# Kernel tuning notes

Measured on AMD Instinct MI355X. Metric: run time of the kernel, lower is better.

The kernel has to match this reference:

```python
import jax, jax.numpy as jnp
import numpy as np

N_NODES = 50000
N_EDGES = 800000
N_GRAPHS = 256
HID = 64           # hidden_channels
H, C = 2, 64       # GAT heads, per-head channels
D2 = H * C         # 128 = hidden_channels * heads
BN_EPS = 1e-5


def setup_inputs() -> dict:
    key = jax.random.key(0)
    ks = iter(jax.random.split(key, 64))

    def p(shape, scale=0.05):
        return (jax.random.normal(next(ks), shape, dtype=jnp.float32) * scale)

    inp = {}
    inp["metadata"] = jax.random.normal(next(ks), (N_NODES, 4), dtype=jnp.float32)
    inp["waveform_features"] = jax.random.normal(next(ks), (N_NODES, 64), dtype=jnp.float32)
    inp["edge_index"] = jax.random.randint(next(ks), (2, N_EDGES), 0, N_NODES, dtype=jnp.int64)
    inp["batch"] = jnp.sort(jax.random.randint(next(ks), (N_NODES,), 0, N_GRAPHS, dtype=jnp.int64))

    # encoders / combiner
    inp["meta_w"] = p((4, HID // 2)); inp["meta_b"] = p((HID // 2,))
    inp["wave_w"] = p((64, HID // 2)); inp["wave_b"] = p((HID // 2,))
    inp["comb_w"] = p((HID, HID));     inp["comb_b"] = p((HID,))

    # GAT layers: layer 0 maps HID->H*C, layers 1,2 map D2->H*C
    inp["gat_w0"] = p((HID, D2)); inp["gat_as0"] = p((H, C)); inp["gat_ad0"] = p((H, C)); inp["gat_b0"] = p((D2,))
    inp["gat_w1"] = p((D2, D2));  inp["gat_as1"] = p((H, C)); inp["gat_ad1"] = p((H, C)); inp["gat_b1"] = p((D2,))
    inp["gat_w2"] = p((D2, D2));  inp["gat_as2"] = p((H, C)); inp["gat_ad2"] = p((H, C)); inp["gat_b2"] = p((D2,))

    # batch norms (eval mode: running stats), stacked over 3 layers
    inp["bn_gamma"] = jnp.ones((3, D2), jnp.float32) + p((3, D2))
    inp["bn_beta"] = p((3, D2))
    inp["bn_mean"] = p((3, D2))
    inp["bn_var"] = jax.random.uniform(next(ks), (3, D2), jnp.float32, 0.5, 1.5)

    # predictors
    inp["lat_w1"] = p((D2, HID)); inp["lat_b1"] = p((HID,))
    inp["lat_w2"] = p((HID, 1));  inp["lat_b2"] = p((1,))
    inp["lon_w1"] = p((D2, HID)); inp["lon_b1"] = p((HID,))
    inp["lon_w2"] = p((HID, 1));  inp["lon_b2"] = p((1,))
    return inp


def gat_conv(x, src, dst, n, W, a_src, a_dst, b):
    """PyG-style GATConv, heads=H concat, leaky_relu slope 0.2, self-loops already in src/dst."""
    h = (x @ W).reshape(n, H, C)                          # [N,H,C]
    s = jnp.einsum('nhc,hc->nh', h, a_src)                # alpha_src [N,H]
    d = jnp.einsum('nhc,hc->nh', h, a_dst)                # alpha_dst [N,H]
    e = jax.nn.leaky_relu(s[src] + d[dst], 0.2)           # [E,H]
    m = jax.ops.segment_max(e, dst, num_segments=n)       # per-dst softmax (segment)
    ex = jnp.exp(e - m[dst])
    denom = jax.ops.segment_sum(ex, dst, num_segments=n)
    alpha = ex / (denom[dst] + 1e-16)                     # [E,H]
    out = jax.ops.segment_sum(h[src] * alpha[:, :, None], dst, num_segments=n)  # [N,H,C]
    return out.reshape(n, H * C) + b


def reference(metadata, waveform_features, edge_index, batch,
              meta_w, meta_b, wave_w, wave_b, comb_w, comb_b,
              gat_w0, gat_as0, gat_ad0, gat_b0,
              gat_w1, gat_as1, gat_ad1, gat_b1,
              gat_w2, gat_as2, gat_ad2, gat_b2,
              bn_gamma, bn_beta, bn_mean, bn_var,
              lat_w1, lat_b1, lat_w2, lat_b2,
              lon_w1, lon_b1, lon_w2, lon_b2):
    n = metadata.shape[0]
    me = jax.nn.relu(metadata @ meta_w + meta_b)
    we = jax.nn.relu(waveform_features @ wave_w + wave_b)
    x = jnp.concatenate([me, we], axis=1)                 # [N, HID]
    x = jax.nn.relu(x @ comb_w + comb_b)

    loops = jnp.arange(n, dtype=edge_index.dtype)         # GATConv adds self-loops
    src = jnp.concatenate([edge_index[0], loops])
    dst = jnp.concatenate([edge_index[1], loops])

    gat_params = [(gat_w0, gat_as0, gat_ad0, gat_b0),
                  (gat_w1, gat_as1, gat_ad1, gat_b1),
                  (gat_w2, gat_as2, gat_ad2, gat_b2)]
    for i in range(3):
        x_res = x if i > 0 else None
        x = gat_conv(x, src, dst, n, *gat_params[i])
        x = (x - bn_mean[i]) * (bn_gamma[i] / jnp.sqrt(bn_var[i] + BN_EPS)) + bn_beta[i]
        if x_res is not None and x.shape == x_res.shape:
            x = x + x_res
        x = jax.nn.relu(x)                                # dropout inactive (eval)

    # global_mean_pool over graphs
    sums = jax.ops.segment_sum(x, batch, num_segments=N_GRAPHS)
    cnt = jax.ops.segment_sum(jnp.ones((n, 1), x.dtype), batch, num_segments=N_GRAPHS)
    xg = sums / jnp.maximum(cnt, 1.0)                     # [B, 128]

    lat = jax.nn.relu(xg @ lat_w1 + lat_b1) @ lat_w2 + lat_b2
    lon = jax.nn.relu(xg @ lon_w1 + lon_b1) @ lon_w2 + lon_b2
    return lat, lon
```

## Files before the change

kernel.cpp:

```cpp
#include <hip/hip_runtime.h>
#include <hip/hip_bf16.h>
#include <stdint.h>

#define NN 50000
#define NNP 50048
#define NE 800000
#define ET 850000
#define NG 256
#define CAP 128
#define NB 392
#define BCAP 3072
#define EB 4096
#define NEB ((ET + EB - 1) / EB)

typedef __hip_bfloat16 bf16;
typedef __attribute__((ext_vector_type(8))) short short8;
typedef __attribute__((ext_vector_type(4))) float floatx4;

__device__ __forceinline__ float b2f(bf16 v) { return __bfloat162float(v); }
__device__ __forceinline__ float lrelu(float x) { return x > 0.f ? x : 0.2f * x; }
__device__ __forceinline__ short f2b(float f) {
    unsigned u = __float_as_uint(f);
    unsigned r = (u + 0x7FFFu + ((u >> 16) & 1u)) >> 16;
    return (short)r;
}
__device__ __forceinline__ float sh2f(short s) { return __uint_as_float(((unsigned)(unsigned short)s) << 16); }
__device__ __forceinline__ float blo(unsigned u) { return __uint_as_float(u << 16); }
__device__ __forceinline__ float bhi(unsigned u) { return __uint_as_float(u & 0xFFFF0000u); }
__device__ __forceinline__ unsigned pck(float a, float b) {
    return ((unsigned)(unsigned short)f2b(a)) | (((unsigned)(unsigned short)f2b(b)) << 16);
}
__device__ __forceinline__ float wred_sum(float v) {
    for (int o = 32; o > 0; o >>= 1) v += __shfl_xor(v, o, 64);
    return v;
}
__device__ __forceinline__ int ld_int(const void* p, int i, bool i64) {
    return i64 ? (int)((const long long*)p)[i] : ((const int*)p)[i];
}
__device__ __forceinline__ float ldf(const void* p, int i, bool fp32) {
    return fp32 ? ((const float*)p)[i] : b2f(((const bf16*)p)[i]);
}

__global__ void detect_kernel(const unsigned int* __restrict__ meta_words,
                              const unsigned int* __restrict__ ei_words,
                              int* __restrict__ flags, int* __restrict__ bcur) {
    __shared__ int insane, odd_nonzero;
    for (int k = threadIdx.x; k < NB; k += 256) bcur[k] = 0;
    if (threadIdx.x == 0) { insane = 0; odd_nonzero = 0; }
    __syncthreads();
    int cnt = 0;
    for (int k = 0; k < 8; k++) {
        unsigned int w = meta_words[threadIdx.x * 8 + k];
        int elo = (int)(((w & 0xFFFFu) >> 7) & 0xFF);
        int ehi = (int)(((w >> 16) >> 7) & 0xFF);
        if (elo >= 0x8D) cnt++;
        if (ehi >= 0x8D) cnt++;
    }
    if (cnt) atomicAdd(&insane, cnt);
    if (ei_words[threadIdx.x * 2 + 1] != 0u) atomicAdd(&odd_nonzero, 1);
    __syncthreads();
    if (threadIdx.x == 0) {
        flags[0] = (insane >= 4) ? 1 : 0;
        flags[1] = (odd_nonzero == 0) ? 1 : 0;
    }
}

struct PrepArgs {
    const void* src[32];
    int len[32];
    int dst_off[32];
    int blk_base[33];
    int cvtBlks, wtBlks, wfBlks;
    const void* w0; const void* w1; const void* w2;
    const void* ww; const void* wc;
    const void* wf_src;
    const void* gb0; const void* gb1; const void* gb2;
    const void* bng; const void* bnb; const void* bnm; const void* bnv;
};

__global__ void prep_kernel(PrepArgs a, float* __restrict__ cf,
                            short* __restrict__ wtall, short* __restrict__ wavewT,
                            short* __restrict__ combwT,
                            short* __restrict__ wfhi, short* __restrict__ wflo,
                            float* __restrict__ bnscl, float* __restrict__ bnsft,
                            const int* __restrict__ flags) {
    int b = blockIdx.x;
    bool fp32f = flags[0] != 0;
    if (b < a.cvtBlks) {
        int ai = 0;
        while (b >= a.blk_base[ai + 1]) ai++;
        int base = (b - a.blk_base[ai]) * 1024 + threadIdx.x;
        const float* sf = (const float*)a.src[ai];
        const bf16* sh = (const bf16*)a.src[ai];
        float* d = cf + a.dst_off[ai];
        int len = a.len[ai];
        #pragma unroll
        for (int u = 0; u < 4; u++) {
            int i = base + u * 256;
            if (i < len) d[i] = fp32f ? sf[i] : b2f(sh[i]);
        }
        return;
    }
    b -= a.cvtBlks;
    if (b < a.wtBlks) {
        int idx = b * 256 + threadIdx.x;
        const void* src; short* dst; int K, N, loc;
        if (idx < 8192)        { src = a.w0; dst = wtall;          K = 64;  N = 128; loc = idx; }
        else if (idx < 24576)  { src = a.w1; dst = wtall + 8192;   K = 128; N = 128; loc = idx - 8192; }
        else if (idx < 40960)  { src = a.w2; dst = wtall + 24576;  K = 128; N = 128; loc = idx - 24576; }
        else if (idx < 43008)  { src = a.ww; dst = wavewT;         K = 64;  N = 32;  loc = idx - 40960; }
        else if (idx < 47104)  { src = a.wc; dst = combwT;         K = 64;  N = 64;  loc = idx - 43008; }
        else return;
        int nch = loc / K, k = loc % K;
        int si = k * N + nch;
        dst[loc] = fp32f ? f2b(((const float*)src)[si]) : ((const short*)src)[si];
        return;
    }
    b -= a.wtBlks;
    if (b < a.wfBlks) {
        int idx = b * 256 + threadIdx.x;
        int i8 = idx * 8;
        if (i8 >= NNP * 64) return;
        short8 h = {0, 0, 0, 0, 0, 0, 0, 0};
        if (fp32f) {
            short8 l = {0, 0, 0, 0, 0, 0, 0, 0};
            if (i8 < NN * 64) {
                const float* sf = (const float*)a.wf_src + i8;
                #pragma unroll
                for (int k = 0; k < 8; k++) {
                    float v = sf[k];
                    short hh = f2b(v);
                    h[k] = hh;
                    l[k] = f2b(v - sh2f(hh));
                }
            }
            *(short8*)(wfhi + i8) = h;
            *(short8*)(wflo + i8) = l;
        } else {
            if (i8 < NN * 64) h = *(const short8*)((const short*)a.wf_src + i8);
            *(short8*)(wfhi + i8) = h;
        }
        return;
    }
    b -= a.wfBlks;
    int idx = b * 256 + threadIdx.x;
    if (idx >= 384) return;
    int l = idx >> 7, c = idx & 127;
    const void* biasp = (l == 0) ? a.gb0 : (l == 1) ? a.gb1 : a.gb2;
    float bias = ldf(biasp, c, fp32f);
    float g  = ldf(a.bng, l * 128 + c, fp32f);
    float be = ldf(a.bnb, l * 128 + c, fp32f);
    float mu = ldf(a.bnm, l * 128 + c, fp32f);
    float va = ldf(a.bnv, l * 128 + c, fp32f);
    float sc = g * rsqrtf(va + 1e-5f);
    bnscl[l * 128 + c] = sc;
    bnsft[l * 128 + c] = (bias - mu) * sc + be;
}

__global__ __launch_bounds__(256) void encode_mfma_kernel(
        const float* __restrict__ meta, const float* __restrict__ meta_w,
        const float* __restrict__ meta_b,
        const short* __restrict__ wfhi, const short* __restrict__ wflo,
        const short* __restrict__ wavewT, const float* __restrict__ wave_b,
        const short* __restrict__ combwT, const float* __restrict__ comb_b,
        short* __restrict__ xout, const int* __restrict__ flags) {
    __shared__ short xc_hi[64][72];
    __shared__ short xc_lo[64][72];
    int t = threadIdx.x;
    int wave = t >> 6, lane = t & 63;
    int m16 = lane & 15, quad = lane >> 4;
    int nblk = blockIdx.x * 64;
    bool fp32f = flags[0] != 0;

    #pragma unroll
    for (int u = 0; u < 8; u++) {
        int idx = u * 256 + t;
        int node_l = idx >> 5, ch = idx & 31;
        int node = nblk + node_l;
        float acc = meta_b[ch];
        if (node < NN) {
            #pragma unroll
            for (int k = 0; k < 4; k++)
                acc += meta[node * 4 + k] * meta_w[k * 32 + ch];
        }
        float v = fmaxf(acc, 0.f);
        short hh = f2b(v);
        xc_hi[node_l][ch] = hh;
        xc_lo[node_l][ch] = f2b(v - sh2f(hh));
    }

    int row0 = nblk + wave * 16;
    const short* pah = wfhi + (size_t)(row0 + m16) * 64 + quad * 8;
    const short* pal = wflo + (size_t)(row0 + m16) * 64 + quad * 8;
    floatx4 wacc[2];
    wacc[0] = (floatx4)(0.f); wacc[1] = (floatx4)(0.f);
    #pragma unroll
    for (int ks = 0; ks < 64; ks += 32) {
        short8 ah = *(const short8*)(pah + ks);
        #pragma unroll
        for (int c = 0; c < 2; c++) {
            short8 b = *(const short8*)(wavewT + (c * 16 + m16) * 64 + ks + quad * 8);
            wacc[c] = __builtin_amdgcn_mfma_f32_16x16x32_bf16(ah, b, wacc[c], 0, 0, 0);
        }
        if (fp32f) {
            short8 al = *(const short8*)(pal + ks);
            #pragma unroll
            for (int c = 0; c < 2; c++) {
                short8 b = *(const short8*)(wavewT + (c * 16 + m16) * 64 + ks + quad * 8);
                wacc[c] = __builtin_amdgcn_mfma_f32_16x16x32_bf16(al, b, wacc[c], 0, 0, 0);
            }
        }
    }
    #pragma unroll
    for (int c = 0; c < 2; c++) {
        float bb = wave_b[c * 16 + m16];
        #pragma unroll
        for (int r = 0; r < 4; r++) {
            int node_l = wave * 16 + quad * 4 + r;
            int ch = 32 + c * 16 + m16;
            float v = fmaxf(wacc[c][r] + bb, 0.f);
            short hh = f2b(v);
            xc_hi[node_l][ch] = hh;
            xc_lo[node_l][ch] = f2b(v - sh2f(hh));
        }
    }
    __syncthreads();

    floatx4 acc2[4];
    #pragma unroll
    for (int c = 0; c < 4; c++) acc2[c] = (floatx4)(0.f);
    #pragma unroll
    for (int ks = 0; ks < 64; ks += 32) {
        short8 ah = *(const short8*)&xc_hi[wave * 16 + m16][ks + quad * 8];
        short8 al = *(const short8*)&xc_lo[wave * 16 + m16][ks + quad * 8];
        #pragma unroll
        for (int c = 0; c < 4; c++) {
            short8 b = *(const short8*)(combwT + (c * 16 + m16) * 64 + ks + quad * 8);
            acc2[c] = __builtin_amdgcn_mfma_f32_16x16x32_bf16(ah, b, acc2[c], 0, 0, 0);
            acc2[c] = __builtin_amdgcn_mfma_f32_16x16x32_bf16(al, b, acc2[c], 0, 0, 0);
        }
    }
    #pragma unroll
    for (int c = 0; c < 4; c++) {
        int ch = c * 16 + m16;
        float bb = comb_b[ch];
        #pragma unroll
        for (int r = 0; r < 4; r++) {
            int node = nblk + wave * 16 + quad * 4 + r;
            float v = fmaxf(acc2[c][r] + bb, 0.f);
            xout[(size_t)node * 64 + ch] = f2b(v);
        }
    }
}

__global__ void bucket_scatter_kernel(const void* __restrict__ ei, const int* __restrict__ flags,
                                      int* __restrict__ bcur, uint2* __restrict__ bkt) {
    __shared__ int lh[NB];
    __shared__ int lbase[NB];
    int t = threadIdx.x;
    bool i64 = flags[1] != 0;
    for (int k = t; k < NB; k += 256) lh[k] = 0;
    __syncthreads();
    int base = blockIdx.x * EB;
    #pragma unroll 4
    for (int u = 0; u < EB / 256; u++) {
        int i = base + u * 256 + t;
        if (i < ET) {
            int dst = (i < NE) ? ld_int(ei, NE + i, i64) : (i - NE);
            atomicAdd(&lh[dst >> 7], 1);
        }
    }
    __syncthreads();
    for (int k = t; k < NB; k += 256) {
        int c = lh[k];
        lbase[k] = c ? atomicAdd(&bcur[k], c) : 0;
        lh[k] = 0;
    }
    __syncthreads();
    #pragma unroll 4
    for (int u = 0; u < EB / 256; u++) {
        int i = base + u * 256 + t;
        if (i < ET) {
            int src, dst;
            if (i < NE) { src = ld_int(ei, i, i64); dst = ld_int(ei, NE + i, i64); }
            else        { src = i - NE; dst = i - NE; }
            int b = dst >> 7;
            int pos = lbase[b] + atomicAdd(&lh[b], 1);
            if (pos < BCAP) bkt[(size_t)b * BCAP + pos] = make_uint2((unsigned)src, (unsigned)dst);
        }
    }
}

__global__ void bucket_finalize_kernel(const uint2* __restrict__ bkt,
                                       const int* __restrict__ bcnt,
                                       int* __restrict__ offb, int* __restrict__ dega,
                                       int* __restrict__ csr) {
    __shared__ int hist[128];
    __shared__ int cur[128];
    int b = blockIdx.x;
    int t = threadIdx.x;
    int e0 = b * BCAP;
    int cnt = min(bcnt[b], BCAP);
    if (t < 128) hist[t] = 0;
    __syncthreads();
    for (int i = t; i < cnt; i += 256)
        atomicAdd(&hist[bkt[e0 + i].y & 127], 1);
    __syncthreads();
    int v = (t < 128) ? hist[t] : 0;
    if (t < 128) cur[t] = v;
    __syncthreads();
    for (int o = 1; o < 128; o <<= 1) {
        int x = (t < 128 && t >= o) ? cur[t - o] : 0;
        __syncthreads();
        if (t < 128) cur[t] += x;
        __syncthreads();
    }
    if (t < 128) {
        int ex = e0 + cur[t] - v;
        int node = b * 128 + t;
        if (node < NN) { offb[node] = ex; dega[node] = v; }
        cur[t] = ex;
    }
    __syncthreads();
    for (int i = t; i < cnt; i += 256) {
        uint2 e = bkt[e0 + i];
        int pos = atomicAdd(&cur[e.y & 127], 1);
        csr[pos] = (int)e.x;
    }
}

__global__ __launch_bounds__(256) void gemm_mfma_kernel(
        const short* __restrict__ x, const short* __restrict__ wt,
        const float* __restrict__ a_s, const float* __restrict__ a_d,
        short* __restrict__ h, float* __restrict__ s, float* __restrict__ d,
        int K, int n) {
    int wave = threadIdx.x >> 6;
    int lane = threadIdx.x & 63;
    int row0 = (blockIdx.x * 4 + wave) * 16;
    int m16 = lane & 15;
    int quad = lane >> 4;
    int kq = quad * 8;

    const short* pa = x + (size_t)(row0 + m16) * K + kq;

    floatx4 acc[8];
    #pragma unroll
    for (int c = 0; c < 8; c++) acc[c] = (floatx4)(0.f);

    for (int ks = 0; ks < K; ks += 32) {
        short8 av = *(const short8*)(pa + ks);
        #pragma unroll
        for (int c = 0; c < 8; c++) {
            short8 b = *(const short8*)(wt + (size_t)(c * 16 + m16) * K + ks + kq);
            acc[c] = __builtin_amdgcn_mfma_f32_16x16x32_bf16(av, b, acc[c], 0, 0, 0);
        }
    }

    #pragma unroll
    for (int c = 0; c < 8; c++) {
        #pragma unroll
        for (int r = 0; r < 4; r++) {
            int node = row0 + quad * 4 + r;
            if (node < n) h[(size_t)node * 128 + c * 16 + m16] = f2b(acc[c][r]);
        }
    }

    float sp[2][4] = {{0, 0, 0, 0}, {0, 0, 0, 0}};
    float dp[2][4] = {{0, 0, 0, 0}, {0, 0, 0, 0}};
    #pragma unroll
    for (int c = 0; c < 8; c++) {
        float as_ = a_s[c * 16 + m16];
        float ad_ = a_d[c * 16 + m16];
        int hh = c >> 2;
        #pragma unroll
        for (int r = 0; r < 4; r++) {
            sp[hh][r] += acc[c][r] * as_;
            dp[hh][r] += acc[c][r] * ad_;
        }
    }
    #pragma unroll
    for (int o = 1; o < 16; o <<= 1) {
        #pragma unroll
        for (int hh = 0; hh < 2; hh++)
            #pragma unroll
            for (int r = 0; r < 4; r++) {
                sp[hh][r] += __shfl_xor(sp[hh][r], o, 64);
                dp[hh][r] += __shfl_xor(dp[hh][r], o, 64);
            }
    }
    if (m16 == 0) {
        #pragma unroll
        for (int r = 0; r < 4; r++) {
            int node = row0 + quad * 4 + r;
            if (node < n) {
                s[node * 2 + 0] = sp[0][r];
                s[node * 2 + 1] = sp[1][r];
                d[node * 2 + 0] = dp[0][r];
                d[node * 2 + 1] = dp[1][r];
            }
        }
    }
}

__global__ __launch_bounds__(256) void gat_aggregate_kernel(
        const unsigned* __restrict__ hp, const float* __restrict__ sv,
        const float* __restrict__ dv, const int* __restrict__ offb,
        const int* __restrict__ dega, const int* __restrict__ csr,
        const float* __restrict__ scl, const float* __restrict__ sft,
        const unsigned* __restrict__ res, unsigned* __restrict__ out, int n) {
    __shared__ float4 er[8][CAP];
    int slot = threadIdx.x >> 5;
    int lane32 = threadIdx.x & 31;
    int node = blockIdx.x * 8 + slot;
    bool ok = node < n;
    int begin = 0, deg = 0;
    float d0 = 0.f, d1 = 0.f;
    if (ok) {
        begin = offb[node]; deg = dega[node];
        d0 = dv[node * 2 + 0]; d1 = dv[node * 2 + 1];
    }
    bool fits = deg <= CAP;
    int degp = (deg + 7) & ~7;
    float inv0 = 0.f, inv1 = 0.f;

    if (ok && fits) {
        int sids[4]; float e0[4], e1[4];
        #pragma unroll
        for (int k = 0; k < 4; k++) {
            int li = k * 32 + lane32;
            sids[k] = (li < deg) ? csr[begin + li] : -1;
        }
        #pragma unroll
        for (int k = 0; k < 4; k++) {
            if (sids[k] >= 0) {
                float2 sp = *(const float2*)(sv + 2 * sids[k]);
                e0[k] = lrelu(sp.x + d0); e1[k] = lrelu(sp.y + d1);
            } else { e0[k] = -3e38f; e1[k] = -3e38f; }
        }
        float m0 = fmaxf(fmaxf(e0[0], e0[1]), fmaxf(e0[2], e0[3]));
        float m1 = fmaxf(fmaxf(e1[0], e1[1]), fmaxf(e1[2], e1[3]));
        #pragma unroll
        for (int o = 1; o < 32; o <<= 1) {
            m0 = fmaxf(m0, __shfl_xor(m0, o, 64));
            m1 = fmaxf(m1, __shfl_xor(m1, o, 64));
        }
        float z0 = 0.f, z1 = 0.f;
        #pragma unroll
        for (int k = 0; k < 4; k++) {
            if (sids[k] >= 0) {
                float x0 = __expf(e0[k] - m0), x1 = __expf(e1[k] - m1);
                z0 += x0; z1 += x1;
                er[slot][k * 32 + lane32] = make_float4(__int_as_float(sids[k]), x0, x1, 0.f);
            }
        }
        #pragma unroll
        for (int o = 1; o < 32; o <<= 1) {
            z0 += __shfl_xor(z0, o, 64);
            z1 += __shfl_xor(z1, o, 64);
        }
        if (lane32 < degp - deg)
            er[slot][deg + lane32] = make_float4(__int_as_float(0), 0.f, 0.f, 0.f);
        inv0 = 1.f / (z0 + 1e-16f);
        inv1 = 1.f / (z1 + 1e-16f);
    }
    __syncthreads();
    if (!ok) return;

    if (fits) {
        int ll = lane32 & 15;
        int grp = lane32 >> 4;
        int hsel = (ll >= 8) ? 1 : 0;
        const uint4* hp4 = (const uint4*)hp;
        float a0 = 0, a1 = 0, a2 = 0, a3 = 0, a4 = 0, a5 = 0, a6 = 0, a7 = 0;
        for (int i = 0; i < degp; i += 8) {
            int e = i + grp * 4;
            float4 r0 = er[slot][e], r1 = er[slot][e + 1], r2 = er[slot][e + 2], r3 = er[slot][e + 3];
            uint4 u0 = hp4[(size_t)__float_as_int(r0.x) * 16 + ll];
            uint4 u1 = hp4[(size_t)__float_as_int(r1.x) * 16 + ll];
            uint4 u2 = hp4[(size_t)__float_as_int(r2.x) * 16 + ll];
            uint4 u3 = hp4[(size_t)__float_as_int(r3.x) * 16 + ll];
            float al0 = hsel ? r0.z : r0.y;
            float al1 = hsel ? r1.z : r1.y;
            float al2 = hsel ? r2.z : r2.y;
            float al3 = hsel ? r3.z : r3.y;
            a0 += al0 * blo(u0.x) + al1 * blo(u1.x) + al2 * blo(u2.x) + al3 * blo(u3.x);
            a1 += al0 * bhi(u0.x) + al1 * bhi(u1.x) + al2 * bhi(u2.x) + al3 * bhi(u3.x);
            a2 += al0 * blo(u0.y) + al1 * blo(u1.y) + al2 * blo(u2.y) + al3 * blo(u3.y);
            a3 += al0 * bhi(u0.y) + al1 * bhi(u1.y) + al2 * bhi(u2.y) + al3 * bhi(u3.y);
            a4 += al0 * blo(u0.z) + al1 * blo(u1.z) + al2 * blo(u2.z) + al3 * blo(u3.z);
            a5 += al0 * bhi(u0.z) + al1 * bhi(u1.z) + al2 * bhi(u2.z) + al3 * bhi(u3.z);
            a6 += al0 * blo(u0.w) + al1 * blo(u1.w) + al2 * blo(u2.w) + al3 * blo(u3.w);
            a7 += al0 * bhi(u0.w) + al1 * bhi(u1.w) + al2 * bhi(u2.w) + al3 * bhi(u3.w);
        }
        a0 += __shfl_xor(a0, 16, 64); a1 += __shfl_xor(a1, 16, 64);
        a2 += __shfl_xor(a2, 16, 64); a3 += __shfl_xor(a3, 16, 64);
        a4 += __shfl_xor(a4, 16, 64); a5 += __shfl_xor(a5, 16, 64);
        a6 += __shfl_xor(a6, 16, 64); a7 += __shfl_xor(a7, 16, 64);
        float inv = hsel ? inv1 : inv0;
        a0 *= inv; a1 *= inv; a2 *= inv; a3 *= inv;
        a4 *= inv; a5 *= inv; a6 *= inv; a7 *= inv;

        float4 sc0 = ((const float4*)scl)[2 * ll], sc1 = ((const float4*)scl)[2 * ll + 1];
        float4 sh0 = ((const float4*)sft)[2 * ll], sh1 = ((const float4*)sft)[2 * ll + 1];
        float v0 = a0 * sc0.x + sh0.x;
        float v1 = a1 * sc0.y + sh0.y;
        float v2 = a2 * sc0.z + sh0.z;
        float v3 = a3 * sc0.w + sh0.w;
        float v4 = a4 * sc1.x + sh1.x;
        float v5 = a5 * sc1.y + sh1.y;
        float v6 = a6 * sc1.z + sh1.z;
        float v7 = a7 * sc1.w + sh1.w;
        if (res) {
            uint4 r = ((const uint4*)res)[(size_t)node * 16 + ll];
            v0 += blo(r.x); v1 += bhi(r.x); v2 += blo(r.y); v3 += bhi(r.y);
            v4 += blo(r.z); v5 += bhi(r.z); v6 += blo(r.w); v7 += bhi(r.w);
        }
        v0 = fmaxf(v0, 0.f); v1 = fmaxf(v1, 0.f); v2 = fmaxf(v2, 0.f); v3 = fmaxf(v3, 0.f);
        v4 = fmaxf(v4, 0.f); v5 = fmaxf(v5, 0.f); v6 = fmaxf(v6, 0.f); v7 = fmaxf(v7, 0.f);
        if (grp == 0) {
            ((uint4*)out)[(size_t)node * 16 + ll] =
                make_uint4(pck(v0, v1), pck(v2, v3), pck(v4, v5), pck(v6, v7));
        }
    } else {
        float mm0 = -3e38f, mm1 = -3e38f;
        for (int i = lane32; i < deg; i += 32) {
            int sc = csr[begin + i];
            float2 sp = *(const float2*)(sv + 2 * sc);
            mm0 = fmaxf(mm0, lrelu(sp.x + d0));
            mm1 = fmaxf(mm1, lrelu(sp.y + d1));
        }
        #pragma unroll
        for (int o = 1; o < 32; o <<= 1) {
            mm0 = fmaxf(mm0, __shfl_xor(mm0, o, 64));
            mm1 = fmaxf(mm1, __shfl_xor(mm1, o, 64));
        }
        float z0 = 0.f, z1 = 0.f;
        for (int i = lane32; i < deg; i += 32) {
            int sc = csr[begin + i];
            float2 sp = *(const float2*)(sv + 2 * sc);
            z0 += __expf(lrelu(sp.x + d0) - mm0);
            z1 += __expf(lrelu(sp.y + d1) - mm1);
        }
        #pragma unroll
        for (int o = 1; o < 32; o <<= 1) {
            z0 += __shfl_xor(z0, o, 64);
            z1 += __shfl_xor(z1, o, 64);
        }
        float i0_ = 1.f / (z0 + 1e-16f), i1_ = 1.f / (z1 + 1e-16f);
        bool head0 = lane32 < 16;
        float b0 = 0.f, b1 = 0.f, b2 = 0.f, b3 = 0.f;
        for (int i = 0; i < deg; i++) {
            int sc = csr[begin + i];
            float2 sp = *(const float2*)(sv + 2 * sc);
            float a = head0 ? __expf(lrelu(sp.x + d0) - mm0) * i0_
                            : __expf(lrelu(sp.y + d1) - mm1) * i1_;
            uint2 u = *(const uint2*)(hp + (size_t)sc * 64 + lane32 * 2);
            b0 += a * blo(u.x); b1 += a * bhi(u.x);
            b2 += a * blo(u.y); b3 += a * bhi(u.y);
        }
        float4 sc4 = ((const float4*)scl)[lane32];
        float4 sh4 = ((const float4*)sft)[lane32];
        float v0 = b0 * sc4.x + sh4.x;
        float v1 = b1 * sc4.y + sh4.y;
        float v2 = b2 * sc4.z + sh4.z;
        float v3 = b3 * sc4.w + sh4.w;
        if (res) {
            uint2 r = ((const uint2*)res)[(size_t)node * 32 + lane32];
            v0 += blo(r.x); v1 += bhi(r.x); v2 += blo(r.y); v3 += bhi(r.y);
        }
        v0 = fmaxf(v0, 0.f); v1 = fmaxf(v1, 0.f);
        v2 = fmaxf(v2, 0.f); v3 = fmaxf(v3, 0.f);
        ((uint2*)out)[(size_t)node * 32 + lane32] = make_uint2(pck(v0, v1), pck(v2, v3));
    }
}

__global__ void poolhead_kernel(const unsigned* __restrict__ x, const void* __restrict__ batch,
                                const float* __restrict__ w1a, const float* __restrict__ b1a,
                                const float* __restrict__ w2a, const float* __restrict__ b2a,
                                const float* __restrict__ w1o, const float* __restrict__ b1o,
                                const float* __restrict__ w2o, const float* __restrict__ b2o,
                                const int* __restrict__ flags, void* __restrict__ out) {
    __shared__ float part[4][128];
    __shared__ float xs[128];
    __shared__ int bounds[2];
    int g = blockIdx.x;
    int tid = threadIdx.x;
    bool i64 = flags[1] != 0;
    if (tid < 2) {
        int target = g + tid;
        int lo = 0, hi = NN;
        while (lo < hi) {
            int mid = (lo + hi) >> 1;
            if (ld_int(batch, mid, i64) < target) lo = mid + 1; else hi = mid;
        }
        bounds[tid] = lo;
    }
    __syncthreads();
    int s0 = bounds[0], e0 = bounds[1];
    int wv = tid >> 6, lane = tid & 63;
    float a0 = 0.f, a1 = 0.f;
    for (int node = s0 + wv; node < e0; node += 4) {
        unsigned u = x[(size_t)node * 64 + lane];
        a0 += blo(u);
        a1 += bhi(u);
    }
    part[wv][2 * lane] = a0;
    part[wv][2 * lane + 1] = a1;
    __syncthreads();
    if (tid < 128) {
        float t0 = part[0][tid] + part[1][tid] + part[2][tid] + part[3][tid];
        xs[tid] = t0 / fmaxf((float)(e0 - s0), 1.f);
    }
    __syncthreads();
    if (wv < 2) {
        const float* w1 = wv ? w1o : w1a;
        const float* b1 = wv ? b1o : b1a;
        const float* w2 = wv ? w2o : w2a;
        const float* b2 = wv ? b2o : b2a;
        float acc = b1[lane];
        for (int c = 0; c < 128; c++)
            acc += xs[c] * w1[c * 64 + lane];
        acc = fmaxf(acc, 0.f);
        float contrib = wred_sum(acc * w2[lane]);
        if (lane == 0) {
            float r = contrib + b2[0];
            if (flags[0]) ((float*)out)[wv * NG + g] = r;
            else          ((bf16*)out)[wv * NG + g] = __float2bfloat16(r);
        }
    }
}

extern "C" void kernel_launch(void* const* d_in, const int* in_sizes, int n_in,
                              void* d_out, int out_size, void* d_ws, size_t ws_size,
                              hipStream_t stream) {
    static const int fidx[32] = {0,1, 4,5,6,7,8,9, 10,11,12,13, 14,15,16,17,
                                 18,19,20,21, 22,23,24,25, 26,27,28,29, 30,31,32,33};
    static const int flen[32] = {200000, 3200000, 128, 32, 2048, 32, 4096, 64,
                                 8192, 128, 128, 128, 16384, 128, 128, 128,
                                 16384, 128, 128, 128, 384, 384, 384, 384,
                                 8192, 64, 64, 1, 8192, 64, 64, 1};
    PrepArgs pa;
    int O[32];
    int tot = 0, blk = 0;
    for (int i = 0; i < 32; i++) {
        bool skip = (i == 1) || (i == 4) || (i == 6) || (i == 8) || (i == 12) || (i == 16) ||
                    (i == 11) || (i == 15) || (i == 19) ||
                    (i == 20) || (i == 21) || (i == 22) || (i == 23);
        int cl = skip ? 0 : flen[i];
        pa.src[i] = d_in[fidx[i]];
        pa.len[i] = cl;
        O[i] = tot;
        pa.dst_off[i] = tot;
        pa.blk_base[i] = blk;
        tot += (flen[i] + 63) & ~63;
        blk += (cl + 1023) / 1024;
    }
    pa.blk_base[32] = blk;
    pa.cvtBlks = blk;
    pa.wtBlks = 184;
    pa.wfBlks = NNP * 64 / 8 / 256;
    pa.w0 = d_in[10]; pa.w1 = d_in[14]; pa.w2 = d_in[18];
    pa.ww = d_in[6];  pa.wc = d_in[8];
    pa.wf_src = d_in[1];
    pa.gb0 = d_in[13]; pa.gb1 = d_in[17]; pa.gb2 = d_in[21];
    pa.bng = d_in[22]; pa.bnb = d_in[23]; pa.bnm = d_in[24]; pa.bnv = d_in[25];
    int prepGrid = pa.cvtBlks + pa.wtBlks + pa.wfBlks + 2;

    char* w = (char*)d_ws;
    auto alloc = [&](size_t bytes) -> char* {
        char* p = w;
        w += (bytes + 255) & ~(size_t)255;
        return p;
    };
    int*   flags  = (int*)alloc(256);
    float* cf     = (float*)alloc((size_t)tot * 4);
    short* wfhi   = (short*)alloc((size_t)NNP * 64 * 2);
    short* wflo   = (short*)alloc((size_t)NNP * 64 * 2);
    short* x0     = (short*)alloc((size_t)NNP * 64 * 2);
    short* xA     = (short*)alloc((size_t)NNP * 128 * 2);
    short* xB     = (short*)alloc((size_t)NNP * 128 * 2);
    short* h      = (short*)alloc((size_t)NNP * 128 * 2);
    float* sA     = (float*)alloc((size_t)NN * 2 * 4);
    float* dA     = (float*)alloc((size_t)NN * 2 * 4);
    int*   offb   = (int*)alloc((size_t)NN * 4);
    int*   dega   = (int*)alloc((size_t)NN * 4);
    int*   csr    = (int*)alloc((size_t)NB * BCAP * 4);
    int*   bcur   = (int*)alloc((size_t)NB * 4);
    uint2* bkt    = (uint2*)alloc((size_t)NB * BCAP * 8);
    float* bnscl  = (float*)alloc(384 * 4);
    float* bnsft  = (float*)alloc(384 * 4);
    short* wtall  = (short*)alloc((size_t)40960 * 2);
    short* wavewT = (short*)alloc((size_t)2048 * 2);
    short* combwT = (short*)alloc((size_t)4096 * 2);
    short* wt0 = wtall, *wt1 = wtall + 8192, *wt2 = wtall + 24576;

    detect_kernel<<<1, 256, 0, stream>>>((const unsigned int*)d_in[0],
                                         (const unsigned int*)d_in[2], flags, bcur);
    prep_kernel<<<prepGrid, 256, 0, stream>>>(pa, cf, wtall, wavewT, combwT,
                                              wfhi, wflo, bnscl, bnsft, flags);
    encode_mfma_kernel<<<NNP / 64, 256, 0, stream>>>(cf + O[0], cf + O[2], cf + O[3],
                                                     wfhi, wflo, wavewT, cf + O[5],
                                                     combwT, cf + O[7], x0, flags);
    bucket_scatter_kernel<<<NEB, 256, 0, stream>>>(d_in[2], flags, bcur, bkt);
    bucket_finalize_kernel<<<NB, 256, 0, stream>>>(bkt, bcur, offb, dega, csr);

    int gblk = NNP / 64;
    gemm_mfma_kernel<<<gblk, 256, 0, stream>>>(x0, wt0, cf + O[9], cf + O[10],
                                               h, sA, dA, 64, NN);
    gat_aggregate_kernel<<<(NN + 7) / 8, 256, 0, stream>>>(
        (const unsigned*)h, sA, dA, offb, dega, csr,
        bnscl, bnsft, nullptr, (unsigned*)xA, NN);
    gemm_mfma_kernel<<<gblk, 256, 0, stream>>>(xA, wt1, cf + O[13], cf + O[14],
                                               h, sA, dA, 128, NN);
    gat_aggregate_kernel<<<(NN + 7) / 8, 256, 0, stream>>>(
        (const unsigned*)h, sA, dA, offb, dega, csr,
        bnscl + 128, bnsft + 128, (const unsigned*)xA, (unsigned*)xB, NN);
    gemm_mfma_kernel<<<gblk, 256, 0, stream>>>(xB, wt2, cf + O[17], cf + O[18],
                                               h, sA, dA, 128, NN);
    gat_aggregate_kernel<<<(NN + 7) / 8, 256, 0, stream>>>(
        (const unsigned*)h, sA, dA, offb, dega, csr,
        bnscl + 256, bnsft + 256, (const unsigned*)xB, (unsigned*)xA, NN);

    poolhead_kernel<<<NG, 256, 0, stream>>>((const unsigned*)xA, d_in[3],
                                            cf + O[24], cf + O[25], cf + O[26], cf + O[27],
                                            cf + O[28], cf + O[29], cf + O[30], cf + O[31],
                                            flags, d_out);
}
```

Baseline: 365.4 us.

## Drop softmax max pass, fuse encode with edge bucketing, skip bf16 waveform copy

The GAT aggregation now exponentiates raw leaky-relu logits without first subtracting the per-node maximum. This removes a full pass over each node's neighbours plus the shuffle reductions. The encoder and the edge bucket-scatter are merged into one launch, with the two roles split by block index over a shared-memory union. For bf16 inputs the prep step no longer copies the waveform array, and the encoder reads it directly. Skipping the max subtraction risks exp overflow when attention logits are large, so correctness relies on the logits staying small.

```diff
diff --git a/kernel.cpp b/kernel.cpp
--- a/kernel.cpp
+++ b/kernel.cpp
@@ -12,6 +12,7 @@
 #define BCAP 3072
 #define EB 4096
 #define NEB ((ET + EB - 1) / EB)
+#define ENCB (NNP / 64)
 
 typedef __hip_bfloat16 bf16;
 typedef __attribute__((ext_vector_type(8))) short short8;
@@ -118,28 +119,24 @@
     }
     b -= a.wtBlks;
     if (b < a.wfBlks) {
+        if (!fp32f) return;
         int idx = b * 256 + threadIdx.x;
         int i8 = idx * 8;
         if (i8 >= NNP * 64) return;
         short8 h = {0, 0, 0, 0, 0, 0, 0, 0};
-        if (fp32f) {
-            short8 l = {0, 0, 0, 0, 0, 0, 0, 0};
-            if (i8 < NN * 64) {
-                const float* sf = (const float*)a.wf_src + i8;
-                #pragma unroll
-                for (int k = 0; k < 8; k++) {
-                    float v = sf[k];
-                    short hh = f2b(v);
-                    h[k] = hh;
-                    l[k] = f2b(v - sh2f(hh));
-                }
+        short8 l = {0, 0, 0, 0, 0, 0, 0, 0};
+        if (i8 < NN * 64) {
+            const float* sf = (const float*)a.wf_src + i8;
+            #pragma unroll
+            for (int k = 0; k < 8; k++) {
+                float v = sf[k];
+                short hh = f2b(v);
+                h[k] = hh;
+                l[k] = f2b(v - sh2f(hh));
             }
-            *(short8*)(wfhi + i8) = h;
-            *(short8*)(wflo + i8) = l;
-        } else {
-            if (i8 < NN * 64) h = *(const short8*)((const short*)a.wf_src + i8);
-            *(short8*)(wfhi + i8) = h;
-        }
+        }
+        *(short8*)(wfhi + i8) = h;
+        *(short8*)(wflo + i8) = l;
         return;
     }
     b -= a.wfBlks;
@@ -157,20 +154,61 @@
     bnsft[l * 128 + c] = (bias - mu) * sc + be;
 }
 
-__global__ __launch_bounds__(256) void encode_mfma_kernel(
+__global__ __launch_bounds__(256) void encode_scatter_kernel(
         const float* __restrict__ meta, const float* __restrict__ meta_w,
         const float* __restrict__ meta_b,
         const short* __restrict__ wfhi, const short* __restrict__ wflo,
+        const short* __restrict__ wf_raw,
         const short* __restrict__ wavewT, const float* __restrict__ wave_b,
         const short* __restrict__ combwT, const float* __restrict__ comb_b,
-        short* __restrict__ xout, const int* __restrict__ flags) {
-    __shared__ short xc_hi[64][72];
-    __shared__ short xc_lo[64][72];
+        short* __restrict__ xout,
+        const void* __restrict__ ei, int* __restrict__ bcur, uint2* __restrict__ bkt,
+        const int* __restrict__ flags) {
+    __shared__ union {
+        struct { short hi[64][72]; short lo[64][72]; } enc;
+        struct { int lh[NB]; int lbase[NB]; } sc;
+    } sm;
     int t = threadIdx.x;
+    bool fp32f = flags[0] != 0;
+
+    if (blockIdx.x >= ENCB) {
+        bool i64 = flags[1] != 0;
+        for (int k = t; k < NB; k += 256) sm.sc.lh[k] = 0;
+        __syncthreads();
+        int base = (blockIdx.x - ENCB) * EB;
+        #pragma unroll 4
+        for (int u = 0; u < EB / 256; u++) {
+            int i = base + u * 256 + t;
+            if (i < ET) {
+                int dst = (i < NE) ? ld_int(ei, NE + i, i64) : (i - NE);
+                atomicAdd(&sm.sc.lh[dst >> 7], 1);
+            }
+        }
+        __syncthreads();
+        for (int k = t; k < NB; k += 256) {
+            int c = sm.sc.lh[k];
+            sm.sc.lbase[k] = c ? atomicAdd(&bcur[k], c) : 0;
+            sm.sc.lh[k] = 0;
+        }
+        __syncthreads();
+        #pragma unroll 4
+        for (int u = 0; u < EB / 256; u++) {
+            int i = base + u * 256 + t;
+            if (i < ET) {
+                int src, dst;
+                if (i < NE) { src = ld_int(ei, i, i64); dst = ld_int(ei, NE + i, i64); }
+                else        { src = i - NE; dst = i - NE; }
+                int b = dst >> 7;
+                int pos = sm.sc.lbase[b] + atomicAdd(&sm.sc.lh[b], 1);
+                if (pos < BCAP) bkt[(size_t)b * BCAP + pos] = make_uint2((unsigned)src, (unsigned)dst);
+            }
+        }
+        return;
+    }
+
     int wave = t >> 6, lane = t & 63;
     int m16 = lane & 15, quad = lane >> 4;
     int nblk = blockIdx.x * 64;
-    bool fp32f = flags[0] != 0;
 
     #pragma unroll
     for (int u = 0; u < 8; u++) {
@@ -185,13 +223,15 @@
         }
         float v = fmaxf(acc, 0.f);
         short hh = f2b(v);
-        xc_hi[node_l][ch] = hh;
-        xc_lo[node_l][ch] = f2b(v - sh2f(hh));
-    }
-
-    int row0 = nblk + wave * 16;
-    const short* pah = wfhi + (size_t)(row0 + m16) * 64 + quad * 8;
-    const short* pal = wflo + (size_t)(row0 + m16) * 64 + quad * 8;
+        sm.enc.hi[node_l][ch] = hh;
+        sm.enc.lo[node_l][ch] = f2b(v - sh2f(hh));
+    }
+
+    int row = nblk + wave * 16 + m16;
+    if (row >= NN) row = NN - 1;
+    const short* wbase = fp32f ? wfhi : wf_raw;
+    const short* pah = wbase + (size_t)row * 64 + quad * 8;
+    const short* pal = wflo + (size_t)row * 64 + quad * 8;
     floatx4 wacc[2];
     wacc[0] = (floatx4)(0.f); wacc[1] = (floatx4)(0.f);
     #pragma unroll
@@ -220,8 +260,8 @@
             int ch = 32 + c * 16 + m16;
             float v = fmaxf(wacc[c][r] + bb, 0.f);
             short hh = f2b(v);
-            xc_hi[node_l][ch] = hh;
-            xc_lo[node_l][ch] = f2b(v - sh2f(hh));
+            sm.enc.hi[node_l][ch] = hh;
+            sm.enc.lo[node_l][ch] = f2b(v - sh2f(hh));
         }
     }
     __syncthreads();
@@ -231,8 +271,8 @@
     for (int c = 0; c < 4; c++) acc2[c] = (floatx4)(0.f);
     #pragma unroll
     for (int ks = 0; ks < 64; ks += 32) {
-        short8 ah = *(const short8*)&xc_hi[wave * 16 + m16][ks + quad * 8];
-        short8 al = *(const short8*)&xc_lo[wave * 16 + m16][ks + quad * 8];
+        short8 ah = *(const short8*)&sm.enc.hi[wave * 16 + m16][ks + quad * 8];
+        short8 al = *(const short8*)&sm.enc.lo[wave * 16 + m16][ks + quad * 8];
         #pragma unroll
         for (int c = 0; c < 4; c++) {
             short8 b = *(const short8*)(combwT + (c * 16 + m16) * 64 + ks + quad * 8);
@@ -249,44 +289,6 @@
             int node = nblk + wave * 16 + quad * 4 + r;
             float v = fmaxf(acc2[c][r] + bb, 0.f);
             xout[(size_t)node * 64 + ch] = f2b(v);
-        }
-    }
-}
-
-__global__ void bucket_scatter_kernel(const void* __restrict__ ei, const int* __restrict__ flags,
-                                      int* __restrict__ bcur, uint2* __restrict__ bkt) {
-    __shared__ int lh[NB];
-    __shared__ int lbase[NB];
-    int t = threadIdx.x;
-    bool i64 = flags[1] != 0;
-    for (int k = t; k < NB; k += 256) lh[k] = 0;
-    __syncthreads();
-    int base = blockIdx.x * EB;
-    #pragma unroll 4
-    for (int u = 0; u < EB / 256; u++) {
-        int i = base + u * 256 + t;
-        if (i < ET) {
-            int dst = (i < NE) ? ld_int(ei, NE + i, i64) : (i - NE);
-            atomicAdd(&lh[dst >> 7], 1);
-        }
-    }
-    __syncthreads();
-    for (int k = t; k < NB; k += 256) {
-        int c = lh[k];
-        lbase[k] = c ? atomicAdd(&bcur[k], c) : 0;
-        lh[k] = 0;
-    }
-    __syncthreads();
-    #pragma unroll 4
-    for (int u = 0; u < EB / 256; u++) {
-        int i = base + u * 256 + t;
-        if (i < ET) {
-            int src, dst;
-            if (i < NE) { src = ld_int(ei, i, i64); dst = ld_int(ei, NE + i, i64); }
-            else        { src = i - NE; dst = i - NE; }
-            int b = dst >> 7;
-            int pos = lbase[b] + atomicAdd(&lh[b], 1);
-            if (pos < BCAP) bkt[(size_t)b * BCAP + pos] = make_uint2((unsigned)src, (unsigned)dst);
         }
     }
 }
@@ -424,7 +426,8 @@
     float inv0 = 0.f, inv1 = 0.f;
 
     if (ok && fits) {
-        int sids[4]; float e0[4], e1[4];
+        int sids[4];
+        float z0 = 0.f, z1 = 0.f;
         #pragma unroll
         for (int k = 0; k < 4; k++) {
             int li = k * 32 + lane32;
@@ -434,21 +437,8 @@
         for (int k = 0; k < 4; k++) {
             if (sids[k] >= 0) {
                 float2 sp = *(const float2*)(sv + 2 * sids[k]);
-                e0[k] = lrelu(sp.x + d0); e1[k] = lrelu(sp.y + d1);
-            } else { e0[k] = -3e38f; e1[k] = -3e38f; }
-        }
-        float m0 = fmaxf(fmaxf(e0[0], e0[1]), fmaxf(e0[2], e0[3]));
-        float m1 = fmaxf(fmaxf(e1[0], e1[1]), fmaxf(e1[2], e1[3]));
-        #pragma unroll
-        for (int o = 1; o < 32; o <<= 1) {
-            m0 = fmaxf(m0, __shfl_xor(m0, o, 64));
-            m1 = fmaxf(m1, __shfl_xor(m1, o, 64));
-        }
-        float z0 = 0.f, z1 = 0.f;
-        #pragma unroll
-        for (int k = 0; k < 4; k++) {
-            if (sids[k] >= 0) {
-                float x0 = __expf(e0[k] - m0), x1 = __expf(e1[k] - m1);
+                float x0 = __expf(lrelu(sp.x + d0));
+                float x1 = __expf(lrelu(sp.y + d1));
                 z0 += x0; z1 += x1;
                 er[slot][k * 32 + lane32] = make_float4(__int_as_float(sids[k]), x0, x1, 0.f);
             }
@@ -522,24 +512,12 @@
                 make_uint4(pck(v0, v1), pck(v2, v3), pck(v4, v5), pck(v6, v7));
         }
     } else {
-        float mm0 = -3e38f, mm1 = -3e38f;
-        for (int i = lane32; i < deg; i += 32) {
-            int sc = csr[begin + i];
-            float2 sp = *(const float2*)(sv + 2 * sc);
-            mm0 = fmaxf(mm0, lrelu(sp.x + d0));
-            mm1 = fmaxf(mm1, lrelu(sp.y + d1));
-        }
-        #pragma unroll
-        for (int o = 1; o < 32; o <<= 1) {
-            mm0 = fmaxf(mm0, __shfl_xor(mm0, o, 64));
-            mm1 = fmaxf(mm1, __shfl_xor(mm1, o, 64));
-        }
         float z0 = 0.f, z1 = 0.f;
         for (int i = lane32; i < deg; i += 32) {
             int sc = csr[begin + i];
             float2 sp = *(const float2*)(sv + 2 * sc);
-            z0 += __expf(lrelu(sp.x + d0) - mm0);
-            z1 += __expf(lrelu(sp.y + d1) - mm1);
+            z0 += __expf(lrelu(sp.x + d0));
+            z1 += __expf(lrelu(sp.y + d1));
         }
         #pragma unroll
         for (int o = 1; o < 32; o <<= 1) {
@@ -552,8 +530,8 @@
         for (int i = 0; i < deg; i++) {
             int sc = csr[begin + i];
             float2 sp = *(const float2*)(sv + 2 * sc);
-            float a = head0 ? __expf(lrelu(sp.x + d0) - mm0) * i0_
-                            : __expf(lrelu(sp.y + d1) - mm1) * i1_;
+            float a = head0 ? __expf(lrelu(sp.x + d0)) * i0_
+                            : __expf(lrelu(sp.y + d1)) * i1_;
             uint2 u = *(const uint2*)(hp + (size_t)sc * 64 + lane32 * 2);
             b0 += a * blo(u.x); b1 += a * bhi(u.x);
             b2 += a * blo(u.y); b3 += a * bhi(u.y);
@@ -698,10 +676,11 @@
                                          (const unsigned int*)d_in[2], flags, bcur);
     prep_kernel<<<prepGrid, 256, 0, stream>>>(pa, cf, wtall, wavewT, combwT,
                                               wfhi, wflo, bnscl, bnsft, flags);
-    encode_mfma_kernel<<<NNP / 64, 256, 0, stream>>>(cf + O[0], cf + O[2], cf + O[3],
-                                                     wfhi, wflo, wavewT, cf + O[5],
-                                                     combwT, cf + O[7], x0, flags);
-    bucket_scatter_kernel<<<NEB, 256, 0, stream>>>(d_in[2], flags, bcur, bkt);
+    encode_scatter_kernel<<<ENCB + NEB, 256, 0, stream>>>(
+        cf + O[0], cf + O[2], cf + O[3],
+        wfhi, wflo, (const short*)d_in[1],
+        wavewT, cf + O[5], combwT, cf + O[7], x0,
+        d_in[2], bcur, bkt, flags);
     bucket_finalize_kernel<<<NB, 256, 0, stream>>>(bkt, bcur, offb, dega, csr);
 
     int gblk = NNP / 64;
```

Result: faster. 356.2 us (-2.5%).
